# Kernel optimization log

Hardware: AMD Instinct MI355X
Metric: run time of the kernel (lower is better)

Reference implementation:

```python
import jax, jax.numpy as jnp
import numpy as np

B, C, H, W = 16, 1, 128, 8192
N_MAX = 128
CHIRP_W, PERIOD = 48, 64
W_OUT = N_MAX * CHIRP_W + (N_MAX - 1)  # 6271 compacted columns (chirps + separators)
SEP_CLASS_ID = 2


def setup_inputs() -> dict:
    key = jax.random.key(0)
    k1, k2, k3, k4 = jax.random.split(key, 4)
    x = jax.random.normal(k1, (B, C, H, W), dtype=jnp.float32)
    starts = jnp.arange(N_MAX, dtype=jnp.int32) * PERIOD
    xi = jnp.stack([starts, starts + CHIRP_W], axis=-1)           # (N_MAX, 2)
    xi = jnp.broadcast_to(xi[None], (B, N_MAX, 2)).astype(jnp.int32)
    N = jax.random.randint(k2, (B,), 96, N_MAX + 1, dtype=jnp.int32)
    N = N.at[0].set(N_MAX)  # pin so static W_OUT equals torch's dynamic int(w_max.max())
    xl = jax.random.randint(k3, (B, W), 0, 2, dtype=jnp.int32)
    sep_param = jax.random.normal(k4, (1, 1, 1), dtype=jnp.float32)
    return {"x": x, "xi": xi, "N": N, "xl": xl, "sep_param": sep_param, "w_out": W_OUT}


def _compactify(x, xi, N, xl, sep_param, w_out):
    """Vectorized TinyBird.compactify_data: remove silence, keep chirp blocks,
    insert one separator column between consecutive valid chirps."""
    Bx, Cx, Hx, Wx = x.shape
    n_max = xi.shape[1]
    idx = jnp.arange(n_max, dtype=jnp.int32)[None, :]             # (1, N_max)
    Nb = N.reshape(-1, 1).astype(jnp.int32)
    valid = idx < Nb                                              # (B, N_max)

    s0, e0 = xi[..., 0], xi[..., 1]
    w = jnp.clip(e0 - s0, 0, None)
    w_valid = jnp.where(valid, w, 0)
    csum = jnp.cumsum(w_valid, axis=1)
    sn = csum - w_valid + idx                                     # new start (seps before = idx)
    en = csum + idx                                               # new end
    xi_new = jnp.where(valid[..., None], jnp.stack([sn, en], -1), 0).astype(xi.dtype)

    BIG = jnp.int32(1 << 30)
    en_srt = jnp.where(valid, en, BIG)                            # strictly increasing over valid part
    t = jnp.arange(w_out, dtype=jnp.int32)[None, :]               # (1, w_out)
    # i = number of chirp ends <= t  ->  chirp whose [sn_i, en_i) may contain t
    i = (en_srt[:, :, None] <= t[:, None, :]).sum(axis=1).astype(jnp.int32)  # (B, w_out)
    ic = jnp.clip(i, 0, n_max - 1)
    take = lambda a: jnp.take_along_axis(a, ic, axis=1)
    sn_i, en_i = take(sn), take(en)
    s0_i, e0_i = take(s0), take(e0)
    in_chirp = (i < Nb) & (t >= sn_i) & (en_i > sn_i) & (e0_i > s0_i)
    src = jnp.clip(s0_i + (t - sn_i), 0, Wx - 1)                  # (B, w_out)

    # separator column: t == en_{i-1}, previous chirp is not the last valid one, en < W
    jp = jnp.clip(i - 1, 0, n_max - 1)
    en_prev = jnp.take_along_axis(en, jp, axis=1)
    is_sep = (i >= 1) & (t == en_prev) & ((i - 1) < (Nb - 1)) & (en_prev < Wx)

    x_g = jnp.take_along_axis(x, src[:, None, None, :], axis=3)   # (B, C, H, w_out)
    sep = sep_param[0, 0, 0]
    x_new = jnp.where(in_chirp[:, None, None, :], x_g,
                      jnp.where(is_sep[:, None, None, :], sep, jnp.float32(0)))
    xl_g = jnp.take_along_axis(xl, src, axis=1)
    xl_new = jnp.where(in_chirp, xl_g,
                       jnp.where(is_sep, jnp.asarray(SEP_CLASS_ID, xl.dtype),
                                 jnp.asarray(0, xl.dtype)))
    return x_new, xi_new, xl_new


def reference(x, xi, N, xl, sep_param, w_out):
    return _compactify(x, xi, N, xl, sep_param, w_out)
```

## Files before the change

### kernel.cpp

```cpp
#include <hip/hip_runtime.h>

#define BB     16
#define HH     128
#define WW     8192
#define N_MAXC 128
#define W_OUTC 6271
#define SEP_CLASS 2.0f

#define X_ELEMS (BB * HH * W_OUTC)
#define XI_OFF  (X_ELEMS)
#define XL_OFF  (X_ELEMS + BB * N_MAXC * 2)

#define MAP_BYTES ((size_t)(BB * W_OUTC) * sizeof(int))


__device__ __forceinline__ void compute_scan(const int* __restrict__ xi, int b, int Nb,
                                             int* s_s0, int* s_e0, int* s_sn, int* s_en,
                                             int tid) {
    if (tid < N_MAXC) {
        s_s0[tid] = xi[(b * N_MAXC + tid) * 2 + 0];
        s_e0[tid] = xi[(b * N_MAXC + tid) * 2 + 1];
    }
    __syncthreads();
    if (tid == 0) {
        int c = 0;
        for (int i = 0; i < N_MAXC; ++i) {
            int w = s_e0[i] - s_s0[i];
            if (w < 0) w = 0;
            int wv = (i < Nb) ? w : 0;
            c += wv;
            s_sn[i] = c - wv + i;
            s_en[i] = c + i;
        }
    }
    __syncthreads();
}

__device__ __forceinline__ int map_col(int t, int Nb,
                                       const int* s_s0, const int* s_e0,
                                       const int* s_sn, const int* s_en) {
    int lo = 0, hi = Nb;
    while (lo < hi) {
        int mid = (lo + hi) >> 1;
        if (s_en[mid] <= t) lo = mid + 1; else hi = mid;
    }
    int i = lo;
    int ic = (i < N_MAXC - 1) ? i : (N_MAXC - 1);
    if (i < Nb) {
        int sn = s_sn[ic], en = s_en[ic];
        if (t >= sn && en > sn && s_e0[ic] > s_s0[ic]) {
            int src = s_s0[ic] + (t - sn);
            src = src < 0 ? 0 : (src > WW - 1 ? WW - 1 : src);
            return src;
        }
    }
    if (i >= 1) {
        int en_prev = s_en[i - 1];
        if (t == en_prev && (i - 1) < (Nb - 1) && en_prev < WW) return -1;
    }
    return -2;
}

#define META_TCOLS 1024

__global__ __launch_bounds__(256) void tb_meta_kernel(const int* __restrict__ xi,
                                                      const int* __restrict__ Nv,
                                                      const int* __restrict__ xl,
                                                      float* __restrict__ out,
                                                      int* __restrict__ map) {
    __shared__ int s_s0[N_MAXC], s_e0[N_MAXC], s_sn[N_MAXC], s_en[N_MAXC];
    const int b   = blockIdx.x;
    const int tid = threadIdx.x;
    const int Nb  = Nv[b];
    compute_scan(xi, b, Nb, s_s0, s_e0, s_sn, s_en, tid);

    if (blockIdx.y == 0 && tid < N_MAXC) {
        const bool valid = tid < Nb;
        out[XI_OFF + (b * N_MAXC + tid) * 2 + 0] = valid ? (float)s_sn[tid] : 0.0f;
        out[XI_OFF + (b * N_MAXC + tid) * 2 + 1] = valid ? (float)s_en[tid] : 0.0f;
    }
    const int t_lo = blockIdx.y * META_TCOLS;
    const int t_hi = (t_lo + META_TCOLS < W_OUTC) ? t_lo + META_TCOLS : W_OUTC;
    for (int t = t_lo + tid; t < t_hi; t += blockDim.x) {
        int m = map_col(t, Nb, s_s0, s_e0, s_sn, s_en);
        if (map) map[b * W_OUTC + t] = m;
        float v;
        if (m >= 0)       v = (float)xl[b * WW + m];
        else if (m == -1) v = SEP_CLASS;
        else              v = 0.0f;
        out[XL_OFF + b * W_OUTC + t] = v;
    }
}

__global__ __launch_bounds__(256) void tb_gather_flat(const float* __restrict__ x,
                                                      const int* __restrict__ map,
                                                      const float* __restrict__ sep_param,
                                                      float* __restrict__ out) {
    const float sep = sep_param[0];
    const unsigned nChunks = (unsigned)(X_ELEMS / 4);
    const unsigned stride  = gridDim.x * blockDim.x;
    for (unsigned c = blockIdx.x * blockDim.x + threadIdx.x; c < nChunks; c += stride) {
        const unsigned flat = c * 4u;
        const unsigned bh   = flat / W_OUTC;
        const unsigned t0   = flat - bh * W_OUTC;
        float4 v;
        float* vv = (float*)&v;
        #pragma unroll
        for (int k = 0; k < 4; ++k) {
            unsigned tk  = t0 + (unsigned)k;
            unsigned bh2 = bh;
            if (tk >= W_OUTC) { tk -= W_OUTC; bh2 = bh + 1; }
            const unsigned b2 = bh2 >> 7;
            const int m = map[b2 * W_OUTC + tk];
            float val;
            if (m >= 0)       val = x[((size_t)bh2 << 13) + (unsigned)m];
            else if (m == -1) val = sep;
            else              val = 0.0f;
            vv[k] = val;
        }
        ((float4*)out)[c] = v;
    }
}

#define TILE   512
#define HCHUNK 32

__global__ __launch_bounds__(256) void tb_gather_tiled(const float* __restrict__ x,
                                                       const int* __restrict__ xi,
                                                       const int* __restrict__ Nv,
                                                       const float* __restrict__ sep_param,
                                                       float* __restrict__ out) {
    __shared__ int s_s0[N_MAXC], s_e0[N_MAXC], s_sn[N_MAXC], s_en[N_MAXC];
    __shared__ int s_map[TILE];
    const int b   = blockIdx.z;
    const int h0  = blockIdx.y * HCHUNK;
    const int t0  = blockIdx.x * TILE;
    const int tid = threadIdx.x;
    const int Nb  = Nv[b];
    compute_scan(xi, b, Nb, s_s0, s_e0, s_sn, s_en, tid);

    for (int j = tid; j < TILE; j += blockDim.x) {
        int t = t0 + j;
        s_map[j] = (t < W_OUTC) ? map_col(t, Nb, s_s0, s_e0, s_sn, s_en) : -2;
    }
    __syncthreads();

    const float sep = sep_param[0];
    const float* xb = x   + (size_t)b * HH * WW;
    float*       ob = out + (size_t)b * HH * W_OUTC;

    for (int r = 0; r < HCHUNK; ++r) {
        const int h = h0 + r;
        const float* xr   = xb + (size_t)h * WW;
        float*       orow = ob + (size_t)h * W_OUTC;
        for (int j = tid; j < TILE; j += blockDim.x) {
            int t = t0 + j;
            if (t < W_OUTC) {
                int m = s_map[j];
                orow[t] = (m >= 0) ? xr[m] : ((m == -1) ? sep : 0.0f);
            }
        }
    }
}

extern "C" void kernel_launch(void* const* d_in, const int* in_sizes, int n_in,
                              void* d_out, int out_size, void* d_ws, size_t ws_size,
                              hipStream_t stream) {
    const float* x   = (const float*)d_in[0];
    const int*   xi  = (const int*)  d_in[1];
    const int*   Nv  = (const int*)  d_in[2];
    const int*   xl  = (const int*)  d_in[3];
    const float* sep = (const float*)d_in[4];
    float*       out = (float*)d_out;

    const bool use_ws = (ws_size >= MAP_BYTES) && (d_ws != nullptr);
    int* map = use_ws ? (int*)d_ws : nullptr;

    tb_meta_kernel<<<dim3(BB, 7), dim3(256), 0, stream>>>(xi, Nv, xl, out, map);

    if (use_ws) {
        tb_gather_flat<<<dim3(2048), dim3(256), 0, stream>>>(x, map, sep, out);
    } else {
        dim3 grid((W_OUTC + TILE - 1) / TILE, HH / HCHUNK, BB);
        tb_gather_tiled<<<grid, dim3(256), 0, stream>>>(x, xi, Nv, sep, out);
    }
}
```

Before: 150.6 us.

## Tile gather kernel with shared-memory column map reused across rows

Replaces the flat grid-stride gather, which reread the map for every element and did per-element div/mod, with a 3D-tiled kernel. Each block loads a 1024-column map slice into shared memory once and reuses it across 16 rows. Loads are made branchless by clamping the source index. The meta kernel now uses a parallel Hillis-Steele scan instead of a single-thread serial scan, and its column tiling changes to 896. Output stores become scalar rather than float4 vector stores, which may lower store efficiency.

Measured after the change: 153.0 us. Within noise of the previous version (+1.6%).

```diff
diff --git a/kernel.cpp b/kernel.cpp
--- a/kernel.cpp
+++ b/kernel.cpp
@@ -13,117 +13,152 @@
 
 #define MAP_BYTES ((size_t)(BB * W_OUTC) * sizeof(int))
 
-
-__device__ __forceinline__ void compute_scan(const int* __restrict__ xi, int b, int Nb,
-                                             int* s_s0, int* s_e0, int* s_sn, int* s_en,
-                                             int tid) {
-    if (tid < N_MAXC) {
-        s_s0[tid] = xi[(b * N_MAXC + tid) * 2 + 0];
-        s_e0[tid] = xi[(b * N_MAXC + tid) * 2 + 1];
-    }
-    __syncthreads();
-    if (tid == 0) {
-        int c = 0;
-        for (int i = 0; i < N_MAXC; ++i) {
-            int w = s_e0[i] - s_s0[i];
-            if (w < 0) w = 0;
-            int wv = (i < Nb) ? w : 0;
-            c += wv;
-            s_sn[i] = c - wv + i;
-            s_en[i] = c + i;
-        }
-    }
-    __syncthreads();
-}
-
-__device__ __forceinline__ int map_col(int t, int Nb,
-                                       const int* s_s0, const int* s_e0,
-                                       const int* s_sn, const int* s_en) {
-    int lo = 0, hi = Nb;
-    while (lo < hi) {
-        int mid = (lo + hi) >> 1;
-        if (s_en[mid] <= t) lo = mid + 1; else hi = mid;
-    }
-    int i = lo;
-    int ic = (i < N_MAXC - 1) ? i : (N_MAXC - 1);
-    if (i < Nb) {
-        int sn = s_sn[ic], en = s_en[ic];
-        if (t >= sn && en > sn && s_e0[ic] > s_s0[ic]) {
-            int src = s_s0[ic] + (t - sn);
-            src = src < 0 ? 0 : (src > WW - 1 ? WW - 1 : src);
-            return src;
-        }
-    }
-    if (i >= 1) {
-        int en_prev = s_en[i - 1];
-        if (t == en_prev && (i - 1) < (Nb - 1) && en_prev < WW) return -1;
-    }
-    return -2;
-}
-
-#define META_TCOLS 1024
-
-__global__ __launch_bounds__(256) void tb_meta_kernel(const int* __restrict__ xi,
-                                                      const int* __restrict__ Nv,
-                                                      const int* __restrict__ xl,
-                                                      float* __restrict__ out,
-                                                      int* __restrict__ map) {
-    __shared__ int s_s0[N_MAXC], s_e0[N_MAXC], s_sn[N_MAXC], s_en[N_MAXC];
+#define TCOLS  1024
+#define HROWS  16
+#define MTILE  896
+
+__global__ __launch_bounds__(256) void tb_meta(const int* __restrict__ xi,
+                                               const int* __restrict__ Nv,
+                                               const int* __restrict__ xl,
+                                               float* __restrict__ out,
+                                               int* __restrict__ map) {
+    __shared__ int s_s0[N_MAXC], s_e0[N_MAXC], s_scan[N_MAXC], s_sn[N_MAXC], s_en[N_MAXC];
     const int b   = blockIdx.x;
     const int tid = threadIdx.x;
     const int Nb  = Nv[b];
-    compute_scan(xi, b, Nb, s_s0, s_e0, s_sn, s_en, tid);
+
+    int wv = 0;
+    if (tid < N_MAXC) {
+        int2 se = ((const int2*)xi)[b * N_MAXC + tid];
+        s_s0[tid] = se.x; s_e0[tid] = se.y;
+        int w = se.y - se.x; if (w < 0) w = 0;
+        wv = (tid < Nb) ? w : 0;
+        s_scan[tid] = wv;
+    }
+    __syncthreads();
+    #pragma unroll
+    for (int off = 1; off < N_MAXC; off <<= 1) {
+        int v = 0;
+        if (tid < N_MAXC && tid >= off) v = s_scan[tid - off];
+        __syncthreads();
+        if (tid < N_MAXC) s_scan[tid] += v;
+        __syncthreads();
+    }
+    if (tid < N_MAXC) {
+        int c = s_scan[tid];
+        s_sn[tid] = c - wv + tid;
+        s_en[tid] = c + tid;
+    }
+    __syncthreads();
 
     if (blockIdx.y == 0 && tid < N_MAXC) {
         const bool valid = tid < Nb;
         out[XI_OFF + (b * N_MAXC + tid) * 2 + 0] = valid ? (float)s_sn[tid] : 0.0f;
         out[XI_OFF + (b * N_MAXC + tid) * 2 + 1] = valid ? (float)s_en[tid] : 0.0f;
     }
-    const int t_lo = blockIdx.y * META_TCOLS;
-    const int t_hi = (t_lo + META_TCOLS < W_OUTC) ? t_lo + META_TCOLS : W_OUTC;
-    for (int t = t_lo + tid; t < t_hi; t += blockDim.x) {
-        int m = map_col(t, Nb, s_s0, s_e0, s_sn, s_en);
+
+    const int t_lo = blockIdx.y * MTILE;
+    const int t_hi = (t_lo + MTILE < W_OUTC) ? t_lo + MTILE : W_OUTC;
+    for (int t = t_lo + tid; t < t_hi; t += 256) {
+        int lo = 0, hi = Nb;
+        while (lo < hi) { int mid = (lo + hi) >> 1; if (s_en[mid] <= t) lo = mid + 1; else hi = mid; }
+        const int i  = lo;
+        const int ic = (i < N_MAXC - 1) ? i : (N_MAXC - 1);
+        int m = -2;
+        if (i < Nb) {
+            int sn = s_sn[ic], en = s_en[ic];
+            if (t >= sn && en > sn && s_e0[ic] > s_s0[ic]) {
+                int src = s_s0[ic] + (t - sn);
+                src = src < 0 ? 0 : (src > WW - 1 ? WW - 1 : src);
+                m = src;
+            }
+        }
+        if (m == -2 && i >= 1) {
+            int ep = s_en[i - 1];
+            if (t == ep && (i - 1) < (Nb - 1) && ep < WW) m = -1;
+        }
         if (map) map[b * W_OUTC + t] = m;
-        float v;
-        if (m >= 0)       v = (float)xl[b * WW + m];
-        else if (m == -1) v = SEP_CLASS;
-        else              v = 0.0f;
+        float v = (m >= 0) ? (float)xl[b * WW + m] : ((m == -1) ? SEP_CLASS : 0.0f);
         out[XL_OFF + b * W_OUTC + t] = v;
     }
 }
 
-__global__ __launch_bounds__(256) void tb_gather_flat(const float* __restrict__ x,
-                                                      const int* __restrict__ map,
-                                                      const float* __restrict__ sep_param,
-                                                      float* __restrict__ out) {
+__global__ __launch_bounds__(256) void tb_gather(const float* __restrict__ x,
+                                                 const int* __restrict__ map,
+                                                 const float* __restrict__ sep_param,
+                                                 float* __restrict__ out) {
+    __shared__ int s_map[TCOLS];
+    const int t0   = blockIdx.x * TCOLS;
+    const int h0   = blockIdx.y * HROWS;
+    const int b    = blockIdx.z;
+    const int tid  = threadIdx.x;
+    const int tmax = W_OUTC - t0;
     const float sep = sep_param[0];
-    const unsigned nChunks = (unsigned)(X_ELEMS / 4);
-    const unsigned stride  = gridDim.x * blockDim.x;
-    for (unsigned c = blockIdx.x * blockDim.x + threadIdx.x; c < nChunks; c += stride) {
-        const unsigned flat = c * 4u;
-        const unsigned bh   = flat / W_OUTC;
-        const unsigned t0   = flat - bh * W_OUTC;
-        float4 v;
-        float* vv = (float*)&v;
-        #pragma unroll
-        for (int k = 0; k < 4; ++k) {
-            unsigned tk  = t0 + (unsigned)k;
-            unsigned bh2 = bh;
-            if (tk >= W_OUTC) { tk -= W_OUTC; bh2 = bh + 1; }
-            const unsigned b2 = bh2 >> 7;
-            const int m = map[b2 * W_OUTC + tk];
-            float val;
-            if (m >= 0)       val = x[((size_t)bh2 << 13) + (unsigned)m];
-            else if (m == -1) val = sep;
-            else              val = 0.0f;
-            vv[k] = val;
-        }
-        ((float4*)out)[c] = v;
-    }
-}
-
-#define TILE   512
-#define HCHUNK 32
+
+    for (int j = tid; j < TCOLS; j += 256) {
+        int t = t0 + j;
+        s_map[j] = (t < W_OUTC) ? map[b * W_OUTC + t] : -2;
+    }
+    __syncthreads();
+
+    const float* xb = x   + (size_t)(b * HH + h0) * WW;
+    float*       ob = out + (size_t)(b * HH + h0) * W_OUTC + t0;
+
+    if (tmax >= TCOLS) {
+        #pragma unroll 4
+        for (int r = 0; r < HROWS; ++r) {
+            const float* xr   = xb + (size_t)r * WW;
+            float*       orow = ob + (size_t)r * W_OUTC;
+            #pragma unroll
+            for (int k = 0; k < 4; ++k) {
+                const int j = k * 256 + tid;
+                const int m = s_map[j];
+                const int a = (m >= 0) ? m : 0;
+                const float xv = xr[a];
+                orow[j] = (m >= 0) ? xv : ((m == -1) ? sep : 0.0f);
+            }
+        }
+    } else {
+        #pragma unroll 4
+        for (int r = 0; r < HROWS; ++r) {
+            const float* xr   = xb + (size_t)r * WW;
+            float*       orow = ob + (size_t)r * W_OUTC;
+            #pragma unroll
+            for (int k = 0; k < 4; ++k) {
+                const int j = k * 256 + tid;
+                if (j < tmax) {
+                    const int m = s_map[j];
+                    const int a = (m >= 0) ? m : 0;
+                    const float xv = xr[a];
+                    orow[j] = (m >= 0) ? xv : ((m == -1) ? sep : 0.0f);
+                }
+            }
+        }
+    }
+}
+
+#define FTILE   512
+#define FHCHUNK 32
+
+__device__ __forceinline__ void fb_scan(const int* __restrict__ xi, int b, int Nb,
+                                        int* s_s0, int* s_e0, int* s_sn, int* s_en, int tid) {
+    if (tid < N_MAXC) {
+        s_s0[tid] = xi[(b * N_MAXC + tid) * 2 + 0];
+        s_e0[tid] = xi[(b * N_MAXC + tid) * 2 + 1];
+    }
+    __syncthreads();
+    if (tid == 0) {
+        int c = 0;
+        for (int i = 0; i < N_MAXC; ++i) {
+            int w = s_e0[i] - s_s0[i]; if (w < 0) w = 0;
+            int wvv = (i < Nb) ? w : 0;
+            c += wvv;
+            s_sn[i] = c - wvv + i;
+            s_en[i] = c + i;
+        }
+    }
+    __syncthreads();
+}
 
 __global__ __launch_bounds__(256) void tb_gather_tiled(const float* __restrict__ x,
                                                        const int* __restrict__ xi,
@@ -131,29 +166,39 @@
                                                        const float* __restrict__ sep_param,
                                                        float* __restrict__ out) {
     __shared__ int s_s0[N_MAXC], s_e0[N_MAXC], s_sn[N_MAXC], s_en[N_MAXC];
-    __shared__ int s_map[TILE];
-    const int b   = blockIdx.z;
-    const int h0  = blockIdx.y * HCHUNK;
-    const int t0  = blockIdx.x * TILE;
-    const int tid = threadIdx.x;
-    const int Nb  = Nv[b];
-    compute_scan(xi, b, Nb, s_s0, s_e0, s_sn, s_en, tid);
-
-    for (int j = tid; j < TILE; j += blockDim.x) {
-        int t = t0 + j;
-        s_map[j] = (t < W_OUTC) ? map_col(t, Nb, s_s0, s_e0, s_sn, s_en) : -2;
-    }
-    __syncthreads();
-
+    __shared__ int s_map[FTILE];
+    const int b = blockIdx.z, h0 = blockIdx.y * FHCHUNK, t0 = blockIdx.x * FTILE;
+    const int tid = threadIdx.x, Nb = Nv[b];
+    fb_scan(xi, b, Nb, s_s0, s_e0, s_sn, s_en, tid);
+    for (int j = tid; j < FTILE; j += 256) {
+        int t = t0 + j, m = -2;
+        if (t < W_OUTC) {
+            int lo = 0, hi = Nb;
+            while (lo < hi) { int mid = (lo + hi) >> 1; if (s_en[mid] <= t) lo = mid + 1; else hi = mid; }
+            int i = lo, ic = (i < N_MAXC - 1) ? i : (N_MAXC - 1);
+            if (i < Nb) {
+                int sn = s_sn[ic], en = s_en[ic];
+                if (t >= sn && en > sn && s_e0[ic] > s_s0[ic]) {
+                    int src = s_s0[ic] + (t - sn);
+                    m = src < 0 ? 0 : (src > WW - 1 ? WW - 1 : src);
+                }
+            }
+            if (m == -2 && i >= 1) {
+                int ep = s_en[i - 1];
+                if (t == ep && (i - 1) < (Nb - 1) && ep < WW) m = -1;
+            }
+        }
+        s_map[j] = m;
+    }
+    __syncthreads();
     const float sep = sep_param[0];
-    const float* xb = x   + (size_t)b * HH * WW;
-    float*       ob = out + (size_t)b * HH * W_OUTC;
-
-    for (int r = 0; r < HCHUNK; ++r) {
+    const float* xb = x + (size_t)b * HH * WW;
+    float* ob = out + (size_t)b * HH * W_OUTC;
+    for (int r = 0; r < FHCHUNK; ++r) {
         const int h = h0 + r;
-        const float* xr   = xb + (size_t)h * WW;
-        float*       orow = ob + (size_t)h * W_OUTC;
-        for (int j = tid; j < TILE; j += blockDim.x) {
+        const float* xr = xb + (size_t)h * WW;
+        float* orow = ob + (size_t)h * W_OUTC;
+        for (int j = tid; j < FTILE; j += 256) {
             int t = t0 + j;
             if (t < W_OUTC) {
                 int m = s_map[j];
@@ -176,12 +221,13 @@
     const bool use_ws = (ws_size >= MAP_BYTES) && (d_ws != nullptr);
     int* map = use_ws ? (int*)d_ws : nullptr;
 
-    tb_meta_kernel<<<dim3(BB, 7), dim3(256), 0, stream>>>(xi, Nv, xl, out, map);
+    tb_meta<<<dim3(BB, 7), dim3(256), 0, stream>>>(xi, Nv, xl, out, map);
 
     if (use_ws) {
-        tb_gather_flat<<<dim3(2048), dim3(256), 0, stream>>>(x, map, sep, out);
+        dim3 grid((W_OUTC + TCOLS - 1) / TCOLS, HH / HROWS, BB);
+        tb_gather<<<grid, dim3(256), 0, stream>>>(x, map, sep, out);
     } else {
-        dim3 grid((W_OUTC + TILE - 1) / TILE, HH / HCHUNK, BB);
+        dim3 grid((W_OUTC + FTILE - 1) / FTILE, HH / FHCHUNK, BB);
         tb_gather_tiled<<<grid, dim3(256), 0, stream>>>(x, xi, Nv, sep, out);
     }
 }
```
